# Kernel tuning notes

Measured on AMD Instinct MI355X. Metric: run time of the kernel, lower is better.

## Reference

```python
import jax, jax.numpy as jnp
import numpy as np

B, S, D, NH = 4, 2048, 768, 12
DK = D // NH  # 64


def setup_inputs() -> dict:
    key = jax.random.key(0)
    ks = jax.random.split(key, 5)
    scale = 1.0 / np.sqrt(D)
    return {
        "x": jax.random.normal(ks[0], (B, S, D), dtype=jnp.float32),
        "Wq": jax.random.normal(ks[1], (D, D), dtype=jnp.float32) * scale,
        "Wk": jax.random.normal(ks[2], (D, D), dtype=jnp.float32) * scale,
        "Wv": jax.random.normal(ks[3], (D, D), dtype=jnp.float32) * scale,
        "W0": jax.random.normal(ks[4], (D, D), dtype=jnp.float32) * scale,
    }


def reference(x, Wq, Wk, Wv, W0):
    b, s, d = x.shape
    # nn.Linear(d, d, bias=False): y = x @ W.T
    q = (x @ Wq.T).reshape(b, s, NH, DK)
    k = (x @ Wk.T).reshape(b, s, NH, DK)
    v = (x @ Wv.T).reshape(b, s, NH, DK)
    scores = jnp.einsum('bqhd,bkhd->bhqk', q, k) / np.sqrt(DK)
    # Faithful to source: softmax over dim=2 (the QUERY axis), no mask.
    attn = jax.nn.softmax(scores, axis=2)
    heads = jnp.einsum('bhqk,bkhd->bhqd', attn, v)
    # Faithful to source: direct reshape (b,h,q,d) -> (b,s,d_m), no transpose.
    out = heads.reshape(b, s, d) @ W0.T
    return out
```

## Files before the change

### kernel.cpp

```cpp
#include <hip/hip_runtime.h>
#include <hip/hip_bf16.h>
#include <stdint.h>
#include <math.h>

#define NB  4
#define NS  2048
#define ND  768
#define NHD 12
#define NDK 64
#define NBH (NB*NHD)

#define QSCALE 0.180336879f

typedef short short8 __attribute__((ext_vector_type(8)));
typedef float f32x4  __attribute__((ext_vector_type(4)));
typedef float f32x16 __attribute__((ext_vector_type(16)));
typedef unsigned int uint2v __attribute__((ext_vector_type(2)));

#define MFMA16(a,b,c) __builtin_amdgcn_mfma_f32_16x16x32_bf16(a,b,c,0,0,0)
#define MFMA32(a,b,c) __builtin_amdgcn_mfma_f32_32x32x16_bf16(a,b,c,0,0,0)

extern "C" __device__ float __ocml_native_exp2_f32(float);
__device__ __forceinline__ float nexp2(float x){ return __ocml_native_exp2_f32(x); }

__device__ __forceinline__ short f2b(float f){
  union { float f; uint32_t u; } v; v.f = f;
  uint32_t u = v.u + 0x7fffu + ((v.u >> 16) & 1u);
  return (short)(u >> 16);
}
__device__ __forceinline__ float b2f(short s){
  union { float f; uint32_t u; } v; v.u = ((uint32_t)(unsigned short)s) << 16; return v.f;
}
__device__ __forceinline__ uint32_t cvtpk(float lo, float hi){
  uint32_t r;
  asm("v_cvt_pk_bf16_f32 %0, %1, %2" : "=v"(r) : "v"(lo), "v"(hi));
  return r;
}
__device__ __forceinline__ short8 mk8(uint32_t a, uint32_t b, uint32_t c, uint32_t d){
  union { uint32_t u[4]; short8 v; } x;
  x.u[0]=a; x.u[1]=b; x.u[2]=c; x.u[3]=d; return x.v;
}
__device__ __forceinline__ void pack2(const float* p, short8& o0, short8& o1){
  uint32_t x0 = cvtpk(p[0], p[1]),  x1 = cvtpk(p[2], p[3]);
  uint32_t y0 = cvtpk(p[4], p[5]),  y1 = cvtpk(p[6], p[7]);
  uint2v r02 = __builtin_amdgcn_permlane32_swap(x0, y0, false, false);
  uint2v r13 = __builtin_amdgcn_permlane32_swap(x1, y1, false, false);
  o0 = mk8(r02.x, r13.x, r02.y, r13.y);
  uint32_t x2 = cvtpk(p[8],  p[9]),  x3 = cvtpk(p[10], p[11]);
  uint32_t y2 = cvtpk(p[12], p[13]), y3 = cvtpk(p[14], p[15]);
  uint2v r46 = __builtin_amdgcn_permlane32_swap(x2, y2, false, false);
  uint2v r57 = __builtin_amdgcn_permlane32_swap(x3, y3, false, false);
  o1 = mk8(r46.x, r57.x, r46.y, r57.y);
}

__device__ __forceinline__ void gload16(const void* g, void* lds){
  __builtin_amdgcn_global_load_lds(
      (const __attribute__((address_space(1))) uint32_t*)g,
      (__attribute__((address_space(3))) uint32_t*)lds, 16, 0, 0);
}

__global__ __launch_bounds__(256) void cast_all(const float* __restrict__ x,
    const float* __restrict__ wq, const float* __restrict__ wk,
    const float* __restrict__ wv, const float* __restrict__ w0,
    short* __restrict__ xb, short* __restrict__ wqb, short* __restrict__ wkb,
    short* __restrict__ wvb, short* __restrict__ w0b){
  const int NX = NB*NS*ND/8;
  const int NW = ND*ND/8;
  int i = blockIdx.x*256 + threadIdx.x;
  const float* src; short* dst; int off;
  if (i < NX){ src = x; dst = xb; off = i; }
  else {
    int j = i - NX; int wsel = j / NW; off = j - wsel*NW;
    src = (wsel==0)?wq:((wsel==1)?wk:((wsel==2)?wv:w0));
    dst = (wsel==0)?wqb:((wsel==1)?wkb:((wsel==2)?wvb:w0b));
  }
  const f32x4* p = (const f32x4*)(src + (size_t)off*8);
  f32x4 v0 = p[0], v1 = p[1];
  short8 r;
  r[0]=f2b(v0[0]); r[1]=f2b(v0[1]); r[2]=f2b(v0[2]); r[3]=f2b(v0[3]);
  r[4]=f2b(v1[0]); r[5]=f2b(v1[1]); r[6]=f2b(v1[2]); r[7]=f2b(v1[3]);
  *(short8*)(dst + (size_t)off*8) = r;
}

__device__ __forceinline__ void gemm128_core(const short* __restrict__ A,
                                             const short* __restrict__ Bw,
                                             int rowA0, int rowB0,
                                             short* As, short* Bs, f32x4 acc[4][4]){
  const int t = threadIdx.x;
  const int l  = t & 63;
  const int wm = ((t >> 7) & 1) * 64;
  const int wn = ((t >> 6) & 1) * 64;
  const int lr = l & 15, lg = l >> 4;
  #pragma unroll
  for (int mt=0; mt<4; ++mt)
    #pragma unroll
    for (int nt=0; nt<4; ++nt) acc[mt][nt] = (f32x4){0.f,0.f,0.f,0.f};

  for (int kt = 0; kt < 12; ++kt){
    #pragma unroll
    for (int c = 0; c < 4; ++c){
      int u  = c*256 + t;
      int m  = u >> 3;
      int kb = ((u & 7) << 4) ^ ((m & 7) << 4);
      gload16((const char*)(A  + (size_t)(rowA0 + m)*768 + kt*64) + kb,
              (char*)As + ((c*256 + (t & 0xC0)) << 4));
      gload16((const char*)(Bw + (size_t)(rowB0 + m)*768 + kt*64) + kb,
              (char*)Bs + ((c*256 + (t & 0xC0)) << 4));
    }
    __syncthreads();
    short8 af[4][2], bf[4][2];
    #pragma unroll
    for (int mt=0; mt<4; ++mt)
      #pragma unroll
      for (int ks=0; ks<2; ++ks){
        int m  = wm + mt*16 + lr;
        int kb = (ks*32 + lg*8) * 2;
        af[mt][ks] = *(const short8*)((const char*)As + ((m*128 + kb) ^ ((m & 7) << 4)));
        int n  = wn + mt*16 + lr;
        bf[mt][ks] = *(const short8*)((const char*)Bs + ((n*128 + kb) ^ ((n & 7) << 4)));
      }
    #pragma unroll
    for (int mt=0; mt<4; ++mt)
      #pragma unroll
      for (int nt=0; nt<4; ++nt){
        acc[mt][nt] = MFMA16(af[mt][0], bf[nt][0], acc[mt][nt]);
        acc[mt][nt] = MFMA16(af[mt][1], bf[nt][1], acc[mt][nt]);
      }
    __syncthreads();
  }
}

__global__ __launch_bounds__(256) void gemm_qkv(const short* __restrict__ Xb,
    const short* __restrict__ Wqb, const short* __restrict__ Wkb, const short* __restrict__ Wvb,
    short* __restrict__ Qf, short* __restrict__ Kf, short* __restrict__ V){
  __shared__ __align__(16) short As[128*64];
  __shared__ __align__(16) short Bs[128*64];
  const int wsel = blockIdx.y / 6;
  const int nb   = (blockIdx.y % 6) * 128;
  const short* W = (wsel==0) ? Wqb : ((wsel==1) ? Wkb : Wvb);
  f32x4 acc[4][4];
  gemm128_core(Xb, W, blockIdx.x*128, nb, As, Bs, acc);
  const int t = threadIdx.x, l = t & 63;
  const int wm = ((t>>7)&1)*64, wn = ((t>>6)&1)*64;
  const int lr = l & 15, lg = l >> 4;
  if (wsel == 2){
    #pragma unroll
    for (int mt=0; mt<4; ++mt)
      #pragma unroll
      for (int nt=0; nt<4; ++nt)
        #pragma unroll
        for (int r=0; r<4; ++r){
          int m = blockIdx.x*128 + wm + mt*16 + lg*4 + r;
          int n = nb + wn + nt*16 + lr;
          V[(size_t)m*768 + n] = f2b(acc[mt][nt][r]);
        }
  } else {
    short* O = (wsel==0) ? Qf : Kf;
    const float scl = (wsel==0) ? QSCALE : 1.0f;
    const int bh = (blockIdx.x >> 4)*NHD + ((nb + wn) >> 6);
    const int s0 = (blockIdx.x & 15)*128 + wm;
    short* Ob = O + (size_t)bh*131072;
    #pragma unroll
    for (int mt=0; mt<4; ++mt)
      #pragma unroll
      for (int nt=0; nt<4; ++nt)
        #pragma unroll
        for (int r=0; r<4; ++r){
          int s  = s0 + mt*16 + lg*4 + r;
          int dk = nt*16 + lr;
          Ob[(size_t)((s>>5)*4 + (dk>>4))*512 + ((dk>>3)&1)*256 + (s&31)*8 + (dk&7)]
            = f2b(acc[mt][nt][r] * scl);
        }
  }
}

__global__ __launch_bounds__(256) void gemm_out(const short* __restrict__ Hb,
    const short* __restrict__ W0b, float* __restrict__ out){
  __shared__ __align__(16) short As[128*64];
  __shared__ __align__(16) short Bs[128*64];
  const int nb = blockIdx.y * 128;
  f32x4 acc[4][4];
  gemm128_core(Hb, W0b, blockIdx.x*128, nb, As, Bs, acc);
  const int t = threadIdx.x, l = t & 63;
  const int wm = ((t>>7)&1)*64, wn = ((t>>6)&1)*64;
  const int lr = l & 15, lg = l >> 4;
  #pragma unroll
  for (int mt=0; mt<4; ++mt)
    #pragma unroll
    for (int nt=0; nt<4; ++nt)
      #pragma unroll
      for (int r=0; r<4; ++r){
        int m = blockIdx.x*128 + wm + mt*16 + lg*4 + r;
        int n = nb + wn + nt*16 + lr;
        out[(size_t)m*768 + n] = acc[mt][nt][r];
      }
}

__global__ __launch_bounds__(256, 3) void pass_a(const short* __restrict__ Qf,
                                                 const short* __restrict__ Kf,
                                                 float* __restrict__ invs){
  __shared__ float redA[2][4][32];
  const int t = threadIdx.x, w = t >> 6, l = t & 63;
  const int lq = l & 31, hf = l >> 5;
  const int linear = blockIdx.y * 32 + blockIdx.x;
  const int c8 = linear & 7, j = linear >> 3;
  const int bh = c8 * 6 + (j >> 5);
  const int kp = j & 31;

  const short8* KgA = (const short8*)(Kf + ((size_t)bh*64 + kp*2    )*2048);
  const short8* KgB = (const short8*)(Kf + ((size_t)bh*64 + kp*2 + 1)*2048);
  short8 kfA[4], kfB[4];
  #pragma unroll
  for (int c=0; c<4; ++c){ kfA[c] = KgA[c*64 + l]; kfB[c] = KgB[c*64 + l]; }

  float psA[16], psB[16];
  #pragma unroll
  for (int r=0; r<16; ++r){ psA[r] = 0.f; psB[r] = 0.f; }

  const short8* Qb = (const short8*)(Qf + (size_t)bh*131072);
  for (int qt = w*16; qt < w*16 + 16; ++qt){
    const short8* Qg = Qb + qt*256;
    short8 q0 = Qg[l], q1 = Qg[64+l], q2 = Qg[128+l], q3 = Qg[192+l];
    {
      f32x16 cA = {};
      cA = MFMA32(kfA[0], q0, cA);
      cA = MFMA32(kfA[1], q1, cA);
      cA = MFMA32(kfA[2], q2, cA);
      cA = MFMA32(kfA[3], q3, cA);
      #pragma unroll
      for (int r=0; r<16; ++r) psA[r] += nexp2(cA[r]);
    }
    {
      f32x16 cB = {};
      cB = MFMA32(kfB[0], q0, cB);
      cB = MFMA32(kfB[1], q1, cB);
      cB = MFMA32(kfB[2], q2, cB);
      cB = MFMA32(kfB[3], q3, cB);
      #pragma unroll
      for (int r=0; r<16; ++r) psB[r] += nexp2(cB[r]);
    }
  }
  #pragma unroll
  for (int r=0; r<16; ++r){
    float a = psA[r], b = psB[r];
    a += __shfl_xor(a, 1); a += __shfl_xor(a, 2);
    a += __shfl_xor(a, 4); a += __shfl_xor(a, 8); a += __shfl_xor(a, 16);
    b += __shfl_xor(b, 1); b += __shfl_xor(b, 2);
    b += __shfl_xor(b, 4); b += __shfl_xor(b, 8); b += __shfl_xor(b, 16);
    if (lq == 0){
      int kr = (r&3) + 8*(r>>2) + 4*hf;
      redA[0][w][kr] = a;
      redA[1][w][kr] = b;
    }
  }
  __syncthreads();
  if (t < 64){
    int kvt = t >> 5, kr = t & 31;
    float s = redA[kvt][0][kr] + redA[kvt][1][kr] + redA[kvt][2][kr] + redA[kvt][3][kr];
    invs[(size_t)bh*NS + (kp*2 + kvt)*32 + kr] = 1.0f / s;
  }
}

__global__ __launch_bounds__(256) void pack_v(const short* __restrict__ V,
                                              const float* __restrict__ invs,
                                              short* __restrict__ Vf){
  __shared__ short tile[64][66];
  const int sb = blockIdx.x * 64;
  const int bh = blockIdx.y;
  const int b = bh / NHD, h = bh % NHD;
  const int t = threadIdx.x;
  {
    int r = t >> 2, dkb = (t & 3) * 16;
    float iv = invs[(size_t)bh*NS + sb + r];
    const short* src = V + ((size_t)(b*NS + sb + r)*NHD + h)*NDK + dkb;
    short8 v0 = *(const short8*)src;
    short8 v1 = *(const short8*)(src + 8);
    #pragma unroll
    for (int j=0;j<8;++j) tile[r][dkb+j]   = f2b(b2f(v0[j]) * iv);
    #pragma unroll
    for (int j=0;j<8;++j) tile[r][dkb+8+j] = f2b(b2f(v1[j]) * iv);
  }
  __syncthreads();
  {
    const int c = t >> 6, l = t & 63;
    const int lq = l & 31, hf = l >> 5;
    const int dk = (c>>1)*32 + lq;
    #pragma unroll
    for (int kt_l = 0; kt_l < 2; ++kt_l){
      int kv0 = kt_l*32 + (c&1)*16 + hf*8;
      short8 o;
      #pragma unroll
      for (int j=0;j<8;++j) o[j] = tile[kv0+j][dk];
      *(short8*)(Vf + (((size_t)bh*64 + (sb>>5) + kt_l)*256 + c*64 + l)*8) = o;
    }
  }
}

__device__ __forceinline__ void reduce_store(float (&red)[2][32][64],
                                             f32x16& a0, f32x16& a1,
                                             int w, int l, int lq, int hf,
                                             short* __restrict__ Hd,
                                             size_t bhNS, int qt){
  if (w >= 2){
    #pragma unroll
    for (int r=0; r<16; ++r){ red[w-2][r][l] = a0[r]; red[w-2][16+r][l] = a1[r]; }
  }
  __syncthreads();
  if (w < 2){
    #pragma unroll
    for (int r=0; r<16; ++r){ a0[r] += red[w][r][l]; a1[r] += red[w][16+r][l]; }
  }
  __syncthreads();
  if (w == 1){
    #pragma unroll
    for (int r=0; r<16; ++r){ red[0][r][l] = a0[r]; red[0][16+r][l] = a1[r]; }
  }
  __syncthreads();
  if (w == 0){
    #pragma unroll
    for (int r=0; r<16; ++r){
      a0[r] += red[0][r][l];
      a1[r] += red[0][16+r][l];
      int q = qt*32 + (r&3) + 8*(r>>2) + 4*hf;
      short* dst = Hd + (bhNS + q)*NDK;
      dst[lq]      = f2b(a0[r]);
      dst[32 + lq] = f2b(a1[r]);
    }
  }
}

__global__ __launch_bounds__(256, 3) void pass_c(const short* __restrict__ Qf,
                                                 const short* __restrict__ Kf,
                                                 const short* __restrict__ Vf,
                                                 short* __restrict__ Hd){
  __shared__ float red[2][32][64];
  const int t = threadIdx.x, w = t >> 6, l = t & 63;
  const int lq = l & 31, hf = l >> 5;
  const int linear = blockIdx.y * 32 + blockIdx.x;
  const int c8 = linear & 7, j = linear >> 3;
  const int bh = c8 * 6 + (j >> 5);
  const int qp = j & 31;

  const short8* QgA = (const short8*)(Qf + ((size_t)bh*64 + qp*2    )*2048);
  const short8* QgB = (const short8*)(Qf + ((size_t)bh*64 + qp*2 + 1)*2048);
  short8 qfA[4], qfB[4];
  #pragma unroll
  for (int c=0; c<4; ++c){ qfA[c] = QgA[c*64 + l]; qfB[c] = QgB[c*64 + l]; }

  const short8* Kb = (const short8*)(Kf + (size_t)bh*131072);
  const short8* Vb = (const short8*)(Vf + (size_t)bh*131072);

  f32x16 accA0 = {}, accA1 = {}, accB0 = {}, accB1 = {};

  for (int kt = w*16; kt < w*16 + 16; ++kt){
    const short8* Kg = Kb + kt*256;
    const short8* Vg = Vb + kt*256;
    short8 k0 = Kg[l], k1 = Kg[64+l], k2 = Kg[128+l], k3 = Kg[192+l];
    short8 v0 = Vg[l], v1 = Vg[64+l], v2 = Vg[128+l], v3 = Vg[192+l];

    {
      f32x16 cA = {};
      cA = MFMA32(k0, qfA[0], cA);
      cA = MFMA32(k1, qfA[1], cA);
      cA = MFMA32(k2, qfA[2], cA);
      cA = MFMA32(k3, qfA[3], cA);
      float pA[16];
      #pragma unroll
      for (int r=0; r<16; ++r) pA[r] = nexp2(cA[r]);
      short8 paA0, paA1;
      pack2(pA, paA0, paA1);
      accA0 = MFMA32(paA0, v0, accA0);
      accA0 = MFMA32(paA1, v1, accA0);
      accA1 = MFMA32(paA0, v2, accA1);
      accA1 = MFMA32(paA1, v3, accA1);
    }
    {
      f32x16 cB = {};
      cB = MFMA32(k0, qfB[0], cB);
      cB = MFMA32(k1, qfB[1], cB);
      cB = MFMA32(k2, qfB[2], cB);
      cB = MFMA32(k3, qfB[3], cB);
      float pB[16];
      #pragma unroll
      for (int r=0; r<16; ++r) pB[r] = nexp2(cB[r]);
      short8 paB0, paB1;
      pack2(pB, paB0, paB1);
      accB0 = MFMA32(paB0, v0, accB0);
      accB0 = MFMA32(paB1, v1, accB0);
      accB1 = MFMA32(paB0, v2, accB1);
      accB1 = MFMA32(paB1, v3, accB1);
    }
  }

  const size_t bhNS = (size_t)bh*NS;
  reduce_store(red, accA0, accA1, w, l, lq, hf, Hd, bhNS, qp*2);
  __syncthreads();
  reduce_store(red, accB0, accB1, w, l, lq, hf, Hd, bhNS, qp*2 + 1);
}

extern "C" void kernel_launch(void* const* d_in, const int* in_sizes, int n_in,
                              void* d_out, int out_size, void* d_ws, size_t ws_size,
                              hipStream_t stream){
  (void)in_sizes; (void)n_in; (void)out_size; (void)ws_size;
  const float* x  = (const float*)d_in[0];
  const float* Wq = (const float*)d_in[1];
  const float* Wk = (const float*)d_in[2];
  const float* Wv = (const float*)d_in[3];
  const float* W0 = (const float*)d_in[4];

  char* ws = (char*)d_ws;
  const size_t SZ_X = (size_t)NB*NS*ND*2;
  const size_t SZ_W = (size_t)ND*ND*2;
  short* Xb   = (short*)(ws);
  short* Wqb  = (short*)(ws + SZ_X);
  short* Wkb  = (short*)(ws + SZ_X + 1*SZ_W);
  short* Wvb  = (short*)(ws + SZ_X + 2*SZ_W);
  short* W0b  = (short*)(ws + SZ_X + 3*SZ_W);
  short* Qf   = (short*)(ws + 1*SZ_X + 4*SZ_W);
  short* Kf   = (short*)(ws + 2*SZ_X + 4*SZ_W);
  short* V    = (short*)(ws + 3*SZ_X + 4*SZ_W);
  short* Vf   = (short*)(ws + 4*SZ_X + 4*SZ_W);
  float* invs = (float*)(ws + 5*SZ_X + 4*SZ_W);
  short* Hd   = Xb;
  float* out  = (float*)d_out;

  cast_all<<<dim3(4224), dim3(256), 0, stream>>>(x, Wq, Wk, Wv, W0,
                                                 Xb, Wqb, Wkb, Wvb, W0b);

  gemm_qkv<<<dim3(64,18), dim3(256), 0, stream>>>(Xb, Wqb, Wkb, Wvb, Qf, Kf, V);
  pass_a<<<dim3(32,48), dim3(256), 0, stream>>>(Qf, Kf, invs);
  pack_v<<<dim3(32,48), dim3(256), 0, stream>>>(V, invs, Vf);
  pass_c<<<dim3(32,48), dim3(256), 0, stream>>>(Qf, Kf, Vf, Hd);
  gemm_out<<<dim3(64,6), dim3(256), 0, stream>>>(Hd, W0b, out);
}
```

Baseline: 180.4 us.

## Double-buffer LDS tiles in GEMM core to prefetch next K-tile

The shared GEMM core used by the QKV projection and output projection kernels now uses two LDS buffers per operand. The first K-tile is loaded before the loop, and each iteration issues the global-to-LDS loads for the next tile before running the MFMAs on the current one. This is meant to hide global load latency behind matrix compute instead of stalling at a barrier every tile. In exchange, LDS use per block doubles to 64KB, which may limit how many blocks fit on a CU at once.

```diff
diff --git a/kernel.cpp b/kernel.cpp
--- a/kernel.cpp
+++ b/kernel.cpp
@@ -96,18 +96,33 @@
     #pragma unroll
     for (int nt=0; nt<4; ++nt) acc[mt][nt] = (f32x4){0.f,0.f,0.f,0.f};
 
+  #pragma unroll
+  for (int c = 0; c < 4; ++c){
+    int u  = c*256 + t;
+    int m  = u >> 3;
+    int kb = ((u & 7) << 4) ^ ((m & 7) << 4);
+    gload16((const char*)(A  + (size_t)(rowA0 + m)*768) + kb,
+            (char*)As + ((c*256 + (t & 0xC0)) << 4));
+    gload16((const char*)(Bw + (size_t)(rowB0 + m)*768) + kb,
+            (char*)Bs + ((c*256 + (t & 0xC0)) << 4));
+  }
+  __syncthreads();
+
   for (int kt = 0; kt < 12; ++kt){
-    #pragma unroll
-    for (int c = 0; c < 4; ++c){
-      int u  = c*256 + t;
-      int m  = u >> 3;
-      int kb = ((u & 7) << 4) ^ ((m & 7) << 4);
-      gload16((const char*)(A  + (size_t)(rowA0 + m)*768 + kt*64) + kb,
-              (char*)As + ((c*256 + (t & 0xC0)) << 4));
-      gload16((const char*)(Bw + (size_t)(rowB0 + m)*768 + kt*64) + kb,
-              (char*)Bs + ((c*256 + (t & 0xC0)) << 4));
-    }
-    __syncthreads();
+    const int cur = (kt & 1) * (128*64);
+    const int nxt = ((kt + 1) & 1) * (128*64);
+    if (kt < 11){
+      #pragma unroll
+      for (int c = 0; c < 4; ++c){
+        int u  = c*256 + t;
+        int m  = u >> 3;
+        int kb = ((u & 7) << 4) ^ ((m & 7) << 4);
+        gload16((const char*)(A  + (size_t)(rowA0 + m)*768 + (kt+1)*64) + kb,
+                (char*)(As + nxt) + ((c*256 + (t & 0xC0)) << 4));
+        gload16((const char*)(Bw + (size_t)(rowB0 + m)*768 + (kt+1)*64) + kb,
+                (char*)(Bs + nxt) + ((c*256 + (t & 0xC0)) << 4));
+      }
+    }
     short8 af[4][2], bf[4][2];
     #pragma unroll
     for (int mt=0; mt<4; ++mt)
@@ -115,9 +130,9 @@
       for (int ks=0; ks<2; ++ks){
         int m  = wm + mt*16 + lr;
         int kb = (ks*32 + lg*8) * 2;
-        af[mt][ks] = *(const short8*)((const char*)As + ((m*128 + kb) ^ ((m & 7) << 4)));
+        af[mt][ks] = *(const short8*)((const char*)(As + cur) + ((m*128 + kb) ^ ((m & 7) << 4)));
         int n  = wn + mt*16 + lr;
-        bf[mt][ks] = *(const short8*)((const char*)Bs + ((n*128 + kb) ^ ((n & 7) << 4)));
+        bf[mt][ks] = *(const short8*)((const char*)(Bs + cur) + ((n*128 + kb) ^ ((n & 7) << 4)));
       }
     #pragma unroll
     for (int mt=0; mt<4; ++mt)
@@ -133,8 +148,8 @@
 __global__ __launch_bounds__(256) void gemm_qkv(const short* __restrict__ Xb,
     const short* __restrict__ Wqb, const short* __restrict__ Wkb, const short* __restrict__ Wvb,
     short* __restrict__ Qf, short* __restrict__ Kf, short* __restrict__ V){
-  __shared__ __align__(16) short As[128*64];
-  __shared__ __align__(16) short Bs[128*64];
+  __shared__ __align__(16) short As[2*128*64];
+  __shared__ __align__(16) short Bs[2*128*64];
   const int wsel = blockIdx.y / 6;
   const int nb   = (blockIdx.y % 6) * 128;
   const short* W = (wsel==0) ? Wqb : ((wsel==1) ? Wkb : Wvb);
@@ -176,8 +191,8 @@
 
 __global__ __launch_bounds__(256) void gemm_out(const short* __restrict__ Hb,
     const short* __restrict__ W0b, float* __restrict__ out){
-  __shared__ __align__(16) short As[128*64];
-  __shared__ __align__(16) short Bs[128*64];
+  __shared__ __align__(16) short As[2*128*64];
+  __shared__ __align__(16) short Bs[2*128*64];
   const int nb = blockIdx.y * 128;
   f32x4 acc[4][4];
   gemm128_core(Hb, W0b, blockIdx.x*128, nb, As, Bs, acc);
```

Measured after the change: 164.9 us. 8.6% less time.
